# Performance work log

Measured on AMD Instinct MI355X. Metric: run time of the kernel, lower is better.

The kernel has to match this reference:

```python
import jax, jax.numpy as jnp
import numpy as np

N = 6144
D_IN = 512
D_OUT = 512
DENSITY = 0.005


def setup_inputs() -> dict:
    key = jax.random.key(0)
    ks = jax.random.split(key, 12)
    x = jax.random.normal(ks[0], (N, D_IN), dtype=jnp.float32)
    adj_a = (jax.random.uniform(ks[1], (N, N)) < DENSITY).astype(jnp.float32)
    adj_b = (jax.random.uniform(ks[2], (N, N)) < DENSITY).astype(jnp.float32)
    # SparseAttention params (xavier-ish scale)
    W_sa = jax.random.normal(ks[3], (D_IN, D_OUT), dtype=jnp.float32) * (1.414 / np.sqrt(D_IN + D_OUT))
    a_sa = jax.random.normal(ks[4], (1, 2 * D_OUT), dtype=jnp.float32) * (1.414 / np.sqrt(1 + 2 * D_OUT))
    # GraphConvolution b params (uniform +-1/sqrt(out))
    stdv = 1.0 / np.sqrt(D_OUT)
    W_gcnb = jax.random.uniform(ks[5], (D_IN, D_OUT), minval=-stdv, maxval=stdv, dtype=jnp.float32)
    b_gcnb = jax.random.uniform(ks[6], (D_OUT,), minval=-stdv, maxval=stdv, dtype=jnp.float32)
    # gate Linear layers: Linear(2*D_IN, 1)
    s = 1.0 / np.sqrt(2 * D_IN)
    Wa = jax.random.uniform(ks[7], (1, 2 * D_IN), minval=-s, maxval=s, dtype=jnp.float32)
    ba = jax.random.uniform(ks[8], (1,), minval=-s, maxval=s, dtype=jnp.float32)
    Wb = jax.random.uniform(ks[9], (1, 2 * D_IN), minval=-s, maxval=s, dtype=jnp.float32)
    bb = jax.random.uniform(ks[10], (1,), minval=-s, maxval=s, dtype=jnp.float32)
    return {"x": x, "adj_a": adj_a, "adj_b": adj_b, "W_sa": W_sa, "a_sa": a_sa,
            "W_gcnb": W_gcnb, "b_gcnb": b_gcnb, "Wa": Wa, "ba": ba, "Wb": Wb, "bb": bb}


def reference(x, adj_a, adj_b, W_sa, a_sa, W_gcnb, b_gcnb, Wa, ba, Wb, bb):
    # type-level gates: sigmoid(Linear(cat[adj@x, x]))
    type_sum_a = adj_a @ x                      # [N, D_IN]
    type_sum_b = adj_b @ x
    attn_a = jax.nn.sigmoid(jnp.concatenate([type_sum_a, x], axis=1) @ Wa.T + ba)  # [N,1]
    attn_b = jax.nn.sigmoid(jnp.concatenate([type_sum_b, x], axis=1) @ Wb.T + bb)

    # SparseAttention over adj_a (edge pattern only)
    h = x @ W_sa                                # [N, D_OUT]
    Hd = h.shape[1]
    s_left = h @ a_sa[0, :Hd]                   # [N] contribution of source node i
    s_right = h @ a_sa[0, Hd:]                  # [N] contribution of target node j
    scores = s_left[:, None] + s_right[None, :]  # [N,N]
    e = jnp.where(adj_a != 0, jnp.exp(-jax.nn.leaky_relu(scores, 0.01)), 0.0)
    attn = e / (jnp.sum(e, axis=1, keepdims=True) + 1e-5)
    x_a = attn @ h                              # [N, D_OUT]

    # GCN branch over adj_b
    x_b = adj_b @ (x @ W_gcnb) + b_gcnb         # [N, D_OUT]

    return jax.nn.sigmoid(attn_a * x_a + attn_b * x_b)
```

## Files before the change

### kernel.cpp

```cpp
#include <hip/hip_runtime.h>
#include <math.h>

#define NN 6144
#define DD 512
#define CAP 128

typedef __bf16 bf16_t;
typedef __bf16 bf16x8 __attribute__((ext_vector_type(8)));
typedef unsigned short u16x8 __attribute__((ext_vector_type(8)));
typedef float f32x4 __attribute__((ext_vector_type(4)));

__device__ __forceinline__ float bf2f(unsigned short u) {
    unsigned v = ((unsigned)u) << 16;
    return __builtin_bit_cast(float, v);
}
__device__ __forceinline__ unsigned short f2bf(float f) {
    unsigned u = __builtin_bit_cast(unsigned, f);
    u += 0x7fffu + ((u >> 16) & 1u);
    return (unsigned short)(u >> 16);
}
__device__ __forceinline__ float sigmoidf_(float z) { return 1.0f / (1.0f + expf(-z)); }

__global__ __launch_bounds__(256) void k_prep(const float* __restrict__ Wsa,
                                              const float* __restrict__ Wg,
                                              const float* __restrict__ x,
                                              const float* __restrict__ Wa,
                                              const float* __restrict__ Wb,
                                              unsigned short* __restrict__ wt,
                                              float* __restrict__ xal, float* __restrict__ xar,
                                              float* __restrict__ xbl, float* __restrict__ xbr) {
    __shared__ float s[64][65];
    int bid = blockIdx.x;
    if (bid < 128) {
        int n0 = (bid & 15) * 64;
        int k0 = (bid >> 4) * 64;
        int tx = threadIdx.x & 63, ty = threadIdx.x >> 6;
        const float* src = (n0 < 512) ? Wsa : Wg;
        int nn0 = n0 & 511;
#pragma unroll
        for (int kk = 0; kk < 64; kk += 4)
            s[kk + ty][tx] = src[(size_t)(k0 + kk + ty) * 512 + nn0 + tx];
        __syncthreads();
#pragma unroll
        for (int nn = 0; nn < 64; nn += 4)
            wt[(size_t)(n0 + nn + ty) * 512 + k0 + tx] = f2bf(s[tx][nn + ty]);
    } else {
        int wave = threadIdx.x >> 6, lane = threadIdx.x & 63;
        int row = (bid - 128) * 4 + wave;
        int k0 = lane * 8;
        const float* xr_ = x + (size_t)row * DD + k0;
        float4 v0 = *(const float4*)xr_;
        float4 v1 = *(const float4*)(xr_ + 4);
        float xv[8] = {v0.x, v0.y, v0.z, v0.w, v1.x, v1.y, v1.z, v1.w};
        float a0 = 0, a1 = 0, b0 = 0, b1 = 0;
#pragma unroll
        for (int j = 0; j < 8; j++) {
            a0 += xv[j] * Wa[k0 + j];
            a1 += xv[j] * Wa[512 + k0 + j];
            b0 += xv[j] * Wb[k0 + j];
            b1 += xv[j] * Wb[512 + k0 + j];
        }
#pragma unroll
        for (int off = 32; off; off >>= 1) {
            a0 += __shfl_down(a0, off); a1 += __shfl_down(a1, off);
            b0 += __shfl_down(b0, off); b1 += __shfl_down(b1, off);
        }
        if (lane == 0) { xal[row] = a0; xar[row] = a1; xbl[row] = b0; xbr[row] = b1; }
    }
}

__global__ __launch_bounds__(256) void k_fused(const float* __restrict__ x,
                                               const bf16_t* __restrict__ wt,
                                               const float* __restrict__ adjA,
                                               const float* __restrict__ adjB,
                                               int* __restrict__ idxA, int* __restrict__ idxB,
                                               int* __restrict__ cntA, int* __restrict__ cntB,
                                               unsigned short* __restrict__ h,
                                               unsigned short* __restrict__ g) {
    int bid = blockIdx.x;
    int wave = threadIdx.x >> 6, lane = threadIdx.x & 63;
    int grp = bid % 3;
    if (grp < 2) {
        int sid = (bid / 3) * 2 + grp;
        int row = sid * 4 + wave;
        int which = row >= NN;
        int r = which ? row - NN : row;
        const float* adj = which ? adjB : adjA;
        int* idx = (which ? idxB : idxA) + (size_t)r * CAP;
        int* cnt = which ? cntB : cntA;

        const float4* arow = (const float4*)(adj + (size_t)r * NN) + lane;
        float4 v[24];
#pragma unroll
        for (int j = 0; j < 24; j++) v[j] = arow[j * 64];

        unsigned m[3] = {0, 0, 0};
#pragma unroll
        for (int j = 0; j < 24; j++) {
            unsigned w_ = (j >> 3);
            unsigned sh = (j & 7) * 4;
            m[w_] |= (v[j].x != 0.f ? 1u : 0u) << sh;
            m[w_] |= (v[j].y != 0.f ? 1u : 0u) << (sh + 1);
            m[w_] |= (v[j].z != 0.f ? 1u : 0u) << (sh + 2);
            m[w_] |= (v[j].w != 0.f ? 1u : 0u) << (sh + 3);
        }
        int c = __popc(m[0]) + __popc(m[1]) + __popc(m[2]);
        int p = c;
#pragma unroll
        for (int off = 1; off < 64; off <<= 1) {
            int t = __shfl_up(p, off);
            if (lane >= off) p += t;
        }
        int pos = p - c;
        int total = __shfl(p, 63);
#pragma unroll
        for (int w_ = 0; w_ < 3; w_++) {
            unsigned mm = m[w_];
            while (mm) {
                int b = __ffs(mm) - 1;
                mm &= mm - 1;
                int e = w_ * 32 + b;
                int col = (e >> 2) * 256 + lane * 4 + (e & 3);
                if (pos < CAP) idx[pos] = col;
                pos++;
            }
        }
        if (lane == 0) cnt[r] = total > CAP ? CAP : total;
    } else {
        int tt = bid / 3;
        int row0 = (tt % (NN / 64)) * 64 + wave * 16;
        int col0 = (tt / (NN / 64)) * 64;
        int lr = lane & 15;
        int kg = (lane >> 4) * 8;

        f32x4 acc[4] = {{0,0,0,0},{0,0,0,0},{0,0,0,0},{0,0,0,0}};
        const float* ap = x + (size_t)(row0 + lr) * DD + kg;
        const bf16_t* bp = wt + (size_t)(col0 + lr) * DD + kg;

        for (int k0 = 0; k0 < DD; k0 += 32) {
            float4 a0 = *(const float4*)(ap + k0);
            float4 a1 = *(const float4*)(ap + k0 + 4);
            u16x8 au;
            au[0] = f2bf(a0.x); au[1] = f2bf(a0.y); au[2] = f2bf(a0.z); au[3] = f2bf(a0.w);
            au[4] = f2bf(a1.x); au[5] = f2bf(a1.y); au[6] = f2bf(a1.z); au[7] = f2bf(a1.w);
            bf16x8 a = __builtin_bit_cast(bf16x8, au);
#pragma unroll
            for (int n = 0; n < 4; n++) {
                bf16x8 b = *(const bf16x8*)(bp + (size_t)n * 16 * DD + k0);
                acc[n] = __builtin_amdgcn_mfma_f32_16x16x32_bf16(a, b, acc[n], 0, 0, 0);
            }
        }
        int dcol = lane & 15;
        int dr0 = (lane >> 4) * 4;
#pragma unroll
        for (int n = 0; n < 4; n++) {
            int col = col0 + n * 16 + dcol;
            unsigned short* dst = (col < 512) ? h : g;
            int cc = col & 511;
#pragma unroll
            for (int r = 0; r < 4; r++) {
                int mr = row0 + dr0 + r;
                dst[(size_t)mr * 512 + cc] = f2bf(acc[n][r]);
            }
        }
    }
}

__global__ __launch_bounds__(256) void k_slr(const unsigned short* __restrict__ h,
                                             const float* __restrict__ a_sa,
                                             float* __restrict__ sl, float* __restrict__ sr) {
    int wave = threadIdx.x >> 6, lane = threadIdx.x & 63;
    int row = blockIdx.x * 4 + wave;
    int k0 = lane * 8;
    uint4 hv = *(const uint4*)(h + (size_t)row * DD + k0);
    unsigned u[4] = {hv.x, hv.y, hv.z, hv.w};
    float s0 = 0, s1 = 0;
#pragma unroll
    for (int j = 0; j < 4; j++) {
        float h0 = bf2f((unsigned short)(u[j] & 0xffff));
        float h1 = bf2f((unsigned short)(u[j] >> 16));
        s0 += h0 * a_sa[k0 + 2 * j] + h1 * a_sa[k0 + 2 * j + 1];
        s1 += h0 * a_sa[512 + k0 + 2 * j] + h1 * a_sa[512 + k0 + 2 * j + 1];
    }
#pragma unroll
    for (int off = 32; off; off >>= 1) { s0 += __shfl_down(s0, off); s1 += __shfl_down(s1, off); }
    if (lane == 0) { sl[row] = s0; sr[row] = s1; }
}

__global__ __launch_bounds__(256) void k_final(
    const int* __restrict__ idxA, const int* __restrict__ cntA,
    const int* __restrict__ idxB, const int* __restrict__ cntB,
    const unsigned short* __restrict__ h, const unsigned short* __restrict__ g,
    const float* __restrict__ sl, const float* __restrict__ sr,
    const float* __restrict__ xal, const float* __restrict__ xar,
    const float* __restrict__ xbl, const float* __restrict__ xbr,
    const float* __restrict__ ba, const float* __restrict__ bb,
    const float* __restrict__ bias, float* __restrict__ out) {
    int i = blockIdx.x;
    int tid = threadIdx.x;
    __shared__ float w[CAP];
    __shared__ int ja[CAP], jb[CAP];
    __shared__ float s_denom, s_ga, s_gb;

    int cA = cntA[i], cB = cntB[i];
    if (tid < cA) {
        int j = idxA[(size_t)i * CAP + tid];
        ja[tid] = j;
        float s = sl[i] + sr[j];
        float lrelu = s > 0.f ? s : 0.01f * s;
        w[tid] = expf(-lrelu);
    }
    if (tid < cB) jb[tid] = idxB[(size_t)i * CAP + tid];
    __syncthreads();

    if (tid < 64) {
        float p = 0.f, gasum = 0.f, gbsum = 0.f;
        for (int t = tid; t < cA; t += 64) { p += w[t]; gasum += xal[ja[t]]; }
        for (int t = tid; t < cB; t += 64) gbsum += xbl[jb[t]];
#pragma unroll
        for (int off = 32; off; off >>= 1) {
            p += __shfl_down(p, off);
            gasum += __shfl_down(gasum, off);
            gbsum += __shfl_down(gbsum, off);
        }
        if (tid == 0) {
            s_denom = p;
            s_ga = sigmoidf_(gasum + xar[i] + ba[0]);
            s_gb = sigmoidf_(gbsum + xbr[i] + bb[0]);
        }
    }
    __syncthreads();
    float inv = 1.f / (s_denom + 1e-5f);
    float ga = s_ga, gb = s_gb;

    int d0 = tid * 2;
    float a0 = 0, a1 = 0, b0 = 0, b1 = 0;
#pragma unroll 4
    for (int t = 0; t < cA; t++) {
        unsigned hv = *(const unsigned*)(h + (size_t)ja[t] * 512 + d0);
        float wt_ = w[t];
        a0 += wt_ * bf2f((unsigned short)(hv & 0xffff));
        a1 += wt_ * bf2f((unsigned short)(hv >> 16));
    }
#pragma unroll 4
    for (int t = 0; t < cB; t++) {
        unsigned gv = *(const unsigned*)(g + (size_t)jb[t] * 512 + d0);
        b0 += bf2f((unsigned short)(gv & 0xffff));
        b1 += bf2f((unsigned short)(gv >> 16));
    }
    float z0 = ga * (a0 * inv) + gb * (b0 + bias[d0]);
    float z1 = ga * (a1 * inv) + gb * (b1 + bias[d0 + 1]);
    out[(size_t)i * 512 + d0]     = sigmoidf_(z0);
    out[(size_t)i * 512 + d0 + 1] = sigmoidf_(z1);
}

extern "C" void kernel_launch(void* const* d_in, const int* in_sizes, int n_in,
                              void* d_out, int out_size, void* d_ws, size_t ws_size,
                              hipStream_t stream) {
    const float* x    = (const float*)d_in[0];
    const float* adjA = (const float*)d_in[1];
    const float* adjB = (const float*)d_in[2];
    const float* Wsa  = (const float*)d_in[3];
    const float* a_sa = (const float*)d_in[4];
    const float* Wg   = (const float*)d_in[5];
    const float* bg   = (const float*)d_in[6];
    const float* Wa   = (const float*)d_in[7];
    const float* ba   = (const float*)d_in[8];
    const float* Wb   = (const float*)d_in[9];
    const float* bb   = (const float*)d_in[10];
    float* out = (float*)d_out;

    char* ws = (char*)d_ws;
    size_t off = 0;
    auto alloc = [&](size_t bytes) -> void* {
        void* p = ws + off;
        off += (bytes + 255) & ~(size_t)255;
        return p;
    };
    unsigned short* wt = (unsigned short*)alloc((size_t)1024 * DD * 2);
    unsigned short* h  = (unsigned short*)alloc((size_t)NN * DD * 2);
    unsigned short* g  = (unsigned short*)alloc((size_t)NN * DD * 2);
    int* idxA = (int*)alloc((size_t)NN * CAP * 4);
    int* idxB = (int*)alloc((size_t)NN * CAP * 4);
    int* cntA = (int*)alloc((size_t)NN * 4);
    int* cntB = (int*)alloc((size_t)NN * 4);
    float* xal = (float*)alloc((size_t)NN * 4);
    float* xar = (float*)alloc((size_t)NN * 4);
    float* xbl = (float*)alloc((size_t)NN * 4);
    float* xbr = (float*)alloc((size_t)NN * 4);
    float* sl = (float*)alloc((size_t)NN * 4);
    float* sr = (float*)alloc((size_t)NN * 4);

    k_prep<<<128 + NN / 4, 256, 0, stream>>>(Wsa, Wg, x, Wa, Wb, wt, xal, xar, xbl, xbr);
    k_fused<<<4608, 256, 0, stream>>>(x, (const bf16_t*)wt, adjA, adjB,
                                      idxA, idxB, cntA, cntB, h, g);
    k_slr<<<NN / 4, 256, 0, stream>>>(h, a_sa, sl, sr);
    k_final<<<NN, 256, 0, stream>>>(idxA, cntA, idxB, cntB, h, g, sl, sr,
                                    xal, xar, xbl, xbr, ba, bb, bg, out);
}
```

Measured before the change: 168.4 us.

## Fold attention score vectors into weights and drop separate score kernel

Precomputes W_sa·a_left and W_sa·a_right in the prep kernel, so the per-row attention scores sl/sr become dot products of x with 512-vectors computed alongside the gate dot products inside the fused kernel. This removes the k_slr launch and its re-read of h, and moves the x-row gate work out of prep into extra blocks of the fused kernel. The adjacency scan also switches to nontemporal integer loads to avoid polluting the cache, and k_final clamps the counts. Scores are now computed from fp32 x and fp32 weights rather than from the bf16-rounded h, which slightly changes numerics.

```diff
diff --git a/kernel.cpp b/kernel.cpp
--- a/kernel.cpp
+++ b/kernel.cpp
@@ -9,6 +9,7 @@
 typedef __bf16 bf16x8 __attribute__((ext_vector_type(8)));
 typedef unsigned short u16x8 __attribute__((ext_vector_type(8)));
 typedef float f32x4 __attribute__((ext_vector_type(4)));
+typedef unsigned u32x4 __attribute__((ext_vector_type(4)));
 
 __device__ __forceinline__ float bf2f(unsigned short u) {
     unsigned v = ((unsigned)u) << 16;
@@ -23,14 +24,12 @@
 
 __global__ __launch_bounds__(256) void k_prep(const float* __restrict__ Wsa,
                                               const float* __restrict__ Wg,
-                                              const float* __restrict__ x,
-                                              const float* __restrict__ Wa,
-                                              const float* __restrict__ Wb,
+                                              const float* __restrict__ a_sa,
                                               unsigned short* __restrict__ wt,
-                                              float* __restrict__ xal, float* __restrict__ xar,
-                                              float* __restrict__ xbl, float* __restrict__ xbr) {
+                                              float* __restrict__ wsl, float* __restrict__ wsr) {
     __shared__ float s[64][65];
     int bid = blockIdx.x;
+    int wave = threadIdx.x >> 6, lane = threadIdx.x & 63;
     if (bid < 128) {
         int n0 = (bid & 15) * 64;
         int k0 = (bid >> 4) * 64;
@@ -45,146 +44,153 @@
         for (int nn = 0; nn < 64; nn += 4)
             wt[(size_t)(n0 + nn + ty) * 512 + k0 + tx] = f2bf(s[tx][nn + ty]);
     } else {
-        int wave = threadIdx.x >> 6, lane = threadIdx.x & 63;
-        int row = (bid - 128) * 4 + wave;
+        int k = (bid - 128) * 4 + wave;
+        int n0 = lane * 8;
+        const float* wr = Wsa + (size_t)k * 512 + n0;
+        float4 w0 = *(const float4*)wr, w1 = *(const float4*)(wr + 4);
+        float4 l0 = *(const float4*)(a_sa + n0), l1 = *(const float4*)(a_sa + n0 + 4);
+        float4 r0 = *(const float4*)(a_sa + 512 + n0), r1 = *(const float4*)(a_sa + 512 + n0 + 4);
+        float sl_ = w0.x*l0.x + w0.y*l0.y + w0.z*l0.z + w0.w*l0.w
+                  + w1.x*l1.x + w1.y*l1.y + w1.z*l1.z + w1.w*l1.w;
+        float sr_ = w0.x*r0.x + w0.y*r0.y + w0.z*r0.z + w0.w*r0.w
+                  + w1.x*r1.x + w1.y*r1.y + w1.z*r1.z + w1.w*r1.w;
+#pragma unroll
+        for (int off = 32; off; off >>= 1) { sl_ += __shfl_down(sl_, off); sr_ += __shfl_down(sr_, off); }
+        if (lane == 0) { wsl[k] = sl_; wsr[k] = sr_; }
+    }
+}
+
+__global__ __launch_bounds__(256) void k_fused(const float* __restrict__ x,
+                                               const bf16_t* __restrict__ wt,
+                                               const float* __restrict__ adjA,
+                                               const float* __restrict__ adjB,
+                                               const float* __restrict__ Wa,
+                                               const float* __restrict__ Wb,
+                                               const float* __restrict__ wsl,
+                                               const float* __restrict__ wsr,
+                                               int* __restrict__ idxA, int* __restrict__ idxB,
+                                               int* __restrict__ cntA, int* __restrict__ cntB,
+                                               unsigned short* __restrict__ h,
+                                               unsigned short* __restrict__ g,
+                                               float* __restrict__ xal, float* __restrict__ xar,
+                                               float* __restrict__ xbl, float* __restrict__ xbr,
+                                               float* __restrict__ sl, float* __restrict__ sr) {
+    int bid = blockIdx.x;
+    int wave = threadIdx.x >> 6, lane = threadIdx.x & 63;
+    if (bid < 4608) {
+        int grp = bid % 3;
+        if (grp < 2) {
+            int sid = (bid / 3) * 2 + grp;
+            int row = sid * 4 + wave;
+            int which = row >= NN;
+            int r = which ? row - NN : row;
+            const float* adj = which ? adjB : adjA;
+            int* idx = (which ? idxB : idxA) + (size_t)r * CAP;
+            int* cnt = which ? cntB : cntA;
+
+            const u32x4* arow = (const u32x4*)(adj + (size_t)r * NN) + lane;
+            u32x4 v[24];
+#pragma unroll
+            for (int j = 0; j < 24; j++) v[j] = __builtin_nontemporal_load(arow + j * 64);
+
+            unsigned m[3] = {0, 0, 0};
+#pragma unroll
+            for (int j = 0; j < 24; j++) {
+                unsigned w_ = (j >> 3);
+                unsigned sh = (j & 7) * 4;
+                m[w_] |= (v[j][0] != 0u ? 1u : 0u) << sh;
+                m[w_] |= (v[j][1] != 0u ? 1u : 0u) << (sh + 1);
+                m[w_] |= (v[j][2] != 0u ? 1u : 0u) << (sh + 2);
+                m[w_] |= (v[j][3] != 0u ? 1u : 0u) << (sh + 3);
+            }
+            int c = __popc(m[0]) + __popc(m[1]) + __popc(m[2]);
+            int p = c;
+#pragma unroll
+            for (int off = 1; off < 64; off <<= 1) {
+                int t = __shfl_up(p, off);
+                if (lane >= off) p += t;
+            }
+            int pos = p - c;
+            int total = __shfl(p, 63);
+#pragma unroll
+            for (int w_ = 0; w_ < 3; w_++) {
+                unsigned mm = m[w_];
+                while (mm) {
+                    int b = __ffs(mm) - 1;
+                    mm &= mm - 1;
+                    int e = w_ * 32 + b;
+                    int col = (e >> 2) * 256 + lane * 4 + (e & 3);
+                    if (pos < CAP) idx[pos] = col;
+                    pos++;
+                }
+            }
+            if (lane == 0) cnt[r] = total > CAP ? CAP : total;
+        } else {
+            int tt = bid / 3;
+            int row0 = (tt % (NN / 64)) * 64 + wave * 16;
+            int col0 = (tt / (NN / 64)) * 64;
+            int lr = lane & 15;
+            int kg = (lane >> 4) * 8;
+
+            f32x4 acc[4] = {{0,0,0,0},{0,0,0,0},{0,0,0,0},{0,0,0,0}};
+            const float* ap = x + (size_t)(row0 + lr) * DD + kg;
+            const bf16_t* bp = wt + (size_t)(col0 + lr) * DD + kg;
+
+            for (int k0 = 0; k0 < DD; k0 += 32) {
+                float4 a0 = *(const float4*)(ap + k0);
+                float4 a1 = *(const float4*)(ap + k0 + 4);
+                u16x8 au;
+                au[0] = f2bf(a0.x); au[1] = f2bf(a0.y); au[2] = f2bf(a0.z); au[3] = f2bf(a0.w);
+                au[4] = f2bf(a1.x); au[5] = f2bf(a1.y); au[6] = f2bf(a1.z); au[7] = f2bf(a1.w);
+                bf16x8 a = __builtin_bit_cast(bf16x8, au);
+#pragma unroll
+                for (int n = 0; n < 4; n++) {
+                    bf16x8 b = *(const bf16x8*)(bp + (size_t)n * 16 * DD + k0);
+                    acc[n] = __builtin_amdgcn_mfma_f32_16x16x32_bf16(a, b, acc[n], 0, 0, 0);
+                }
+            }
+            int dcol = lane & 15;
+            int dr0 = (lane >> 4) * 4;
+#pragma unroll
+            for (int n = 0; n < 4; n++) {
+                int col = col0 + n * 16 + dcol;
+                unsigned short* dst = (col < 512) ? h : g;
+                int cc = col & 511;
+#pragma unroll
+                for (int rr = 0; rr < 4; rr++) {
+                    int mr = row0 + dr0 + rr;
+                    dst[(size_t)mr * 512 + cc] = f2bf(acc[n][rr]);
+                }
+            }
+        }
+    } else {
+        int pid = bid - 4608;
+        int row = pid * 4 + wave;
         int k0 = lane * 8;
         const float* xr_ = x + (size_t)row * DD + k0;
         float4 v0 = *(const float4*)xr_;
         float4 v1 = *(const float4*)(xr_ + 4);
         float xv[8] = {v0.x, v0.y, v0.z, v0.w, v1.x, v1.y, v1.z, v1.w};
-        float a0 = 0, a1 = 0, b0 = 0, b1 = 0;
-#pragma unroll
-        for (int j = 0; j < 8; j++) {
-            a0 += xv[j] * Wa[k0 + j];
-            a1 += xv[j] * Wa[512 + k0 + j];
-            b0 += xv[j] * Wb[k0 + j];
-            b1 += xv[j] * Wb[512 + k0 + j];
-        }
-#pragma unroll
-        for (int off = 32; off; off >>= 1) {
-            a0 += __shfl_down(a0, off); a1 += __shfl_down(a1, off);
-            b0 += __shfl_down(b0, off); b1 += __shfl_down(b1, off);
-        }
-        if (lane == 0) { xal[row] = a0; xar[row] = a1; xbl[row] = b0; xbr[row] = b1; }
-    }
-}
-
-__global__ __launch_bounds__(256) void k_fused(const float* __restrict__ x,
-                                               const bf16_t* __restrict__ wt,
-                                               const float* __restrict__ adjA,
-                                               const float* __restrict__ adjB,
-                                               int* __restrict__ idxA, int* __restrict__ idxB,
-                                               int* __restrict__ cntA, int* __restrict__ cntB,
-                                               unsigned short* __restrict__ h,
-                                               unsigned short* __restrict__ g) {
-    int bid = blockIdx.x;
-    int wave = threadIdx.x >> 6, lane = threadIdx.x & 63;
-    int grp = bid % 3;
-    if (grp < 2) {
-        int sid = (bid / 3) * 2 + grp;
-        int row = sid * 4 + wave;
-        int which = row >= NN;
-        int r = which ? row - NN : row;
-        const float* adj = which ? adjB : adjA;
-        int* idx = (which ? idxB : idxA) + (size_t)r * CAP;
-        int* cnt = which ? cntB : cntA;
-
-        const float4* arow = (const float4*)(adj + (size_t)r * NN) + lane;
-        float4 v[24];
-#pragma unroll
-        for (int j = 0; j < 24; j++) v[j] = arow[j * 64];
-
-        unsigned m[3] = {0, 0, 0};
-#pragma unroll
-        for (int j = 0; j < 24; j++) {
-            unsigned w_ = (j >> 3);
-            unsigned sh = (j & 7) * 4;
-            m[w_] |= (v[j].x != 0.f ? 1u : 0u) << sh;
-            m[w_] |= (v[j].y != 0.f ? 1u : 0u) << (sh + 1);
-            m[w_] |= (v[j].z != 0.f ? 1u : 0u) << (sh + 2);
-            m[w_] |= (v[j].w != 0.f ? 1u : 0u) << (sh + 3);
-        }
-        int c = __popc(m[0]) + __popc(m[1]) + __popc(m[2]);
-        int p = c;
-#pragma unroll
-        for (int off = 1; off < 64; off <<= 1) {
-            int t = __shfl_up(p, off);
-            if (lane >= off) p += t;
-        }
-        int pos = p - c;
-        int total = __shfl(p, 63);
-#pragma unroll
-        for (int w_ = 0; w_ < 3; w_++) {
-            unsigned mm = m[w_];
-            while (mm) {
-                int b = __ffs(mm) - 1;
-                mm &= mm - 1;
-                int e = w_ * 32 + b;
-                int col = (e >> 2) * 256 + lane * 4 + (e & 3);
-                if (pos < CAP) idx[pos] = col;
-                pos++;
-            }
-        }
-        if (lane == 0) cnt[r] = total > CAP ? CAP : total;
-    } else {
-        int tt = bid / 3;
-        int row0 = (tt % (NN / 64)) * 64 + wave * 16;
-        int col0 = (tt / (NN / 64)) * 64;
-        int lr = lane & 15;
-        int kg = (lane >> 4) * 8;
-
-        f32x4 acc[4] = {{0,0,0,0},{0,0,0,0},{0,0,0,0},{0,0,0,0}};
-        const float* ap = x + (size_t)(row0 + lr) * DD + kg;
-        const bf16_t* bp = wt + (size_t)(col0 + lr) * DD + kg;
-
-        for (int k0 = 0; k0 < DD; k0 += 32) {
-            float4 a0 = *(const float4*)(ap + k0);
-            float4 a1 = *(const float4*)(ap + k0 + 4);
-            u16x8 au;
-            au[0] = f2bf(a0.x); au[1] = f2bf(a0.y); au[2] = f2bf(a0.z); au[3] = f2bf(a0.w);
-            au[4] = f2bf(a1.x); au[5] = f2bf(a1.y); au[6] = f2bf(a1.z); au[7] = f2bf(a1.w);
-            bf16x8 a = __builtin_bit_cast(bf16x8, au);
-#pragma unroll
-            for (int n = 0; n < 4; n++) {
-                bf16x8 b = *(const bf16x8*)(bp + (size_t)n * 16 * DD + k0);
-                acc[n] = __builtin_amdgcn_mfma_f32_16x16x32_bf16(a, b, acc[n], 0, 0, 0);
-            }
-        }
-        int dcol = lane & 15;
-        int dr0 = (lane >> 4) * 4;
-#pragma unroll
-        for (int n = 0; n < 4; n++) {
-            int col = col0 + n * 16 + dcol;
-            unsigned short* dst = (col < 512) ? h : g;
-            int cc = col & 511;
-#pragma unroll
-            for (int r = 0; r < 4; r++) {
-                int mr = row0 + dr0 + r;
-                dst[(size_t)mr * 512 + cc] = f2bf(acc[n][r]);
-            }
-        }
-    }
-}
-
-__global__ __launch_bounds__(256) void k_slr(const unsigned short* __restrict__ h,
-                                             const float* __restrict__ a_sa,
-                                             float* __restrict__ sl, float* __restrict__ sr) {
-    int wave = threadIdx.x >> 6, lane = threadIdx.x & 63;
-    int row = blockIdx.x * 4 + wave;
-    int k0 = lane * 8;
-    uint4 hv = *(const uint4*)(h + (size_t)row * DD + k0);
-    unsigned u[4] = {hv.x, hv.y, hv.z, hv.w};
-    float s0 = 0, s1 = 0;
-#pragma unroll
-    for (int j = 0; j < 4; j++) {
-        float h0 = bf2f((unsigned short)(u[j] & 0xffff));
-        float h1 = bf2f((unsigned short)(u[j] >> 16));
-        s0 += h0 * a_sa[k0 + 2 * j] + h1 * a_sa[k0 + 2 * j + 1];
-        s1 += h0 * a_sa[512 + k0 + 2 * j] + h1 * a_sa[512 + k0 + 2 * j + 1];
-    }
-#pragma unroll
-    for (int off = 32; off; off >>= 1) { s0 += __shfl_down(s0, off); s1 += __shfl_down(s1, off); }
-    if (lane == 0) { sl[row] = s0; sr[row] = s1; }
+        float d[6] = {0, 0, 0, 0, 0, 0};
+        const float* srcs[6] = {Wa + k0, Wa + 512 + k0, Wb + k0, Wb + 512 + k0, wsl + k0, wsr + k0};
+#pragma unroll
+        for (int q = 0; q < 6; q++) {
+            float4 w0 = *(const float4*)srcs[q];
+            float4 w1 = *(const float4*)(srcs[q] + 4);
+            float wv[8] = {w0.x, w0.y, w0.z, w0.w, w1.x, w1.y, w1.z, w1.w};
+#pragma unroll
+            for (int j = 0; j < 8; j++) d[q] += xv[j] * wv[j];
+        }
+#pragma unroll
+        for (int off = 32; off; off >>= 1)
+#pragma unroll
+            for (int q = 0; q < 6; q++) d[q] += __shfl_down(d[q], off);
+        if (lane == 0) {
+            xal[row] = d[0]; xar[row] = d[1];
+            xbl[row] = d[2]; xbr[row] = d[3];
+            sl[row] = d[4]; sr[row] = d[5];
+        }
+    }
 }
 
 __global__ __launch_bounds__(256) void k_final(
@@ -202,7 +208,8 @@
     __shared__ int ja[CAP], jb[CAP];
     __shared__ float s_denom, s_ga, s_gb;
 
-    int cA = cntA[i], cB = cntB[i];
+    int cA = cntA[i]; cA = cA > CAP ? CAP : cA;
+    int cB = cntB[i]; cB = cB > CAP ? CAP : cB;
     if (tid < cA) {
         int j = idxA[(size_t)i * CAP + tid];
         ja[tid] = j;
@@ -288,13 +295,15 @@
     float* xar = (float*)alloc((size_t)NN * 4);
     float* xbl = (float*)alloc((size_t)NN * 4);
     float* xbr = (float*)alloc((size_t)NN * 4);
-    float* sl = (float*)alloc((size_t)NN * 4);
-    float* sr = (float*)alloc((size_t)NN * 4);
-
-    k_prep<<<128 + NN / 4, 256, 0, stream>>>(Wsa, Wg, x, Wa, Wb, wt, xal, xar, xbl, xbr);
-    k_fused<<<4608, 256, 0, stream>>>(x, (const bf16_t*)wt, adjA, adjB,
-                                      idxA, idxB, cntA, cntB, h, g);
-    k_slr<<<NN / 4, 256, 0, stream>>>(h, a_sa, sl, sr);
+    float* sl  = (float*)alloc((size_t)NN * 4);
+    float* sr  = (float*)alloc((size_t)NN * 4);
+    float* wsl = (float*)alloc((size_t)DD * 4);
+    float* wsr = (float*)alloc((size_t)DD * 4);
+
+    k_prep<<<256, 256, 0, stream>>>(Wsa, Wg, a_sa, wt, wsl, wsr);
+    k_fused<<<6144, 256, 0, stream>>>(x, (const bf16_t*)wt, adjA, adjB, Wa, Wb, wsl, wsr,
+                                      idxA, idxB, cntA, cntB, h, g,
+                                      xal, xar, xbl, xbr, sl, sr);
     k_final<<<NN, 256, 0, stream>>>(idxA, cntA, idxB, cntB, h, g, sl, sr,
                                     xal, xar, xbl, xbr, ba, bb, bg, out);
 }
```

Measured after the change: 164.8 us. 1.02x faster.
